# Performance work log

Measured on AMD Instinct MI355X. Metric: run time of the kernel, lower is better.

The kernel has to match this reference:

```python
import jax, jax.numpy as jnp
import numpy as np

LOCAL_RANGE = 7  # module default local_range
NUM_HEADS = 8


def setup_inputs() -> dict:
    key = jax.random.key(0)
    k1, k2, k3 = jax.random.split(key, 3)
    B, S, D = 2, 2048, 512
    hidden_states = jax.random.normal(k1, (B, S, D), dtype=jnp.float32)
    scale = 1.0 / (D ** 0.5)
    Wq = jax.random.normal(k2, (D, D), dtype=jnp.float32) * scale
    Wk = jax.random.normal(k3, (D, D), dtype=jnp.float32) * scale
    return {"hidden_states": hidden_states, "Wq": Wq, "Wk": Wk}


def reference(hidden_states, Wq, Wk):
    B, S, D = hidden_states.shape
    H = NUM_HEADS
    dh = D // H
    # inner attention: only attn_weights matter (context_layer is overwritten)
    q = (hidden_states @ Wq).reshape(B, S, H, dh).transpose(0, 2, 1, 3)  # [B,H,S,dh]
    k = (hidden_states @ Wk).reshape(B, S, H, dh).transpose(0, 2, 1, 3)  # [B,H,S,dh]
    scores = jnp.einsum('bhid,bhjd->bhij', q, k) / (dh ** 0.5)          # [B,H,S,S]
    attn_weights = jax.nn.softmax(scores, axis=-1)
    # band-diagonal local mask: |i-j| <= local_range (vectorized form of the python loop)
    idx = jnp.arange(S)
    band = (jnp.abs(idx[:, None] - idx[None, :]) <= LOCAL_RANGE).astype(attn_weights.dtype)  # [S,S]
    local_w = attn_weights * band
    local_w = local_w / (jnp.sum(local_w, axis=-1, keepdims=True) + 1e-6)
    # context = matmul(local_attn_weights, hidden_states): per-head contraction
    context = jnp.einsum('bhij,bjd->bhid', local_w, hidden_states)       # [B,H,S,D]
    return context
```

## Files before the change

### kernel.cpp

```cpp
#include <hip/hip_runtime.h>
#include <hip/hip_bf16.h>
#include <math.h>

#define SEQ   2048
#define DIM   512
#define NH    8
#define DH    64
#define LR    7
#define TI    8
#define NROW  (TI + 2 * LR)

typedef __bf16 bf16_t;
typedef __bf16 bf16x8 __attribute__((ext_vector_type(8)));
typedef float  f32x4  __attribute__((ext_vector_type(4)));

typedef __attribute__((address_space(3))) void  lds_void;
typedef __attribute__((address_space(1))) const void gbl_cvoid;

__global__ __launch_bounds__(256) void prep(
    const float* __restrict__ hs,
    const float* __restrict__ Wq, const float* __restrict__ Wk,
    bf16_t* __restrict__ hsb,
    bf16_t* __restrict__ Wt)
{
    const int tid = threadIdx.x;
    const int bx  = blockIdx.x;

    if (bx < 1024) {
        const size_t base = ((size_t)bx * 256 + tid) * 8;
        const float4 f0 = *(const float4*)(hs + base);
        const float4 f1 = *(const float4*)(hs + base + 4);
        union { bf16_t b[8]; uint4 u; } cv;
        cv.b[0]=(bf16_t)f0.x; cv.b[1]=(bf16_t)f0.y; cv.b[2]=(bf16_t)f0.z; cv.b[3]=(bf16_t)f0.w;
        cv.b[4]=(bf16_t)f1.x; cv.b[5]=(bf16_t)f1.y; cv.b[6]=(bf16_t)f1.z; cv.b[7]=(bf16_t)f1.w;
        *(uint4*)(hsb + base) = cv.u;
        return;
    }

    __shared__ float tile[64][68];
    const int t  = bx - 1024;
    const int k0 = (t & 7) * 64;
    const int n0 = (t >> 3) * 64;
    const float* W = (n0 < DIM) ? Wq : Wk;
    const int nn0 = n0 & (DIM - 1);

    #pragma unroll
    for (int ph = 0; ph < 4; ++ph) {
        const int kk = ph * 16 + (tid >> 4);
        const int nn = (tid & 15) * 4;
        const float4 v = *(const float4*)(W + (size_t)(k0 + kk) * DIM + nn0 + nn);
        tile[kk][nn + 0] = v.x; tile[kk][nn + 1] = v.y;
        tile[kk][nn + 2] = v.z; tile[kk][nn + 3] = v.w;
    }
    __syncthreads();
    #pragma unroll
    for (int ph = 0; ph < 4; ++ph) {
        const int nn = ph * 16 + (tid >> 4);
        const int kk = (tid & 15) * 4;
        union { bf16_t b[4]; ushort4 u; } cv;
        #pragma unroll
        for (int u = 0; u < 4; ++u) cv.b[u] = (bf16_t)tile[kk + u][nn];
        *(ushort4*)(Wt + (size_t)(n0 + nn) * DIM + k0 + kk) = cv.u;
    }
}

__global__ __launch_bounds__(256) void qk_gemm_v5(
    const bf16_t* __restrict__ A,
    const bf16_t* __restrict__ Bt,
    bf16_t* __restrict__ C)
{
    __shared__ bf16_t As[128 * 128];
    __shared__ bf16_t Bs[128 * 128];

    const int tid  = threadIdx.x;
    const int wave = tid >> 6;
    const int lane = tid & 63;
    const int l15  = lane & 15;
    const int quad = lane >> 4;
    const int wm   = (wave >> 1) * 64;
    const int wn_  = (wave & 1) * 64;
    const int m0   = blockIdx.x * 128;
    const int n0   = blockIdx.y * 128;

    f32x4 acc[4][4] = {};

    for (int kt = 0; kt < 4; ++kt) {
        const int k0 = kt * 128;
        #pragma unroll
        for (int g = 0; g < 8; ++g) {
            const int ra = wave * 32 + g * 4 + quad;
            const int cg = (l15 ^ (ra & 15)) * 8;
            __builtin_amdgcn_global_load_lds(
                (gbl_cvoid*)(A + (size_t)(m0 + ra) * DIM + k0 + cg),
                (lds_void*)(As + (wave * 32 + g * 4) * 128), 16, 0, 0);
            __builtin_amdgcn_global_load_lds(
                (gbl_cvoid*)(Bt + (size_t)(n0 + ra) * DIM + k0 + cg),
                (lds_void*)(Bs + (wave * 32 + g * 4) * 128), 16, 0, 0);
        }
        __syncthreads();

        #pragma unroll
        for (int s = 0; s < 4; ++s) {
            const int cs = ((s * 4 + quad) ^ l15) * 8;
            bf16x8 af[4], bfv[4];
            #pragma unroll
            for (int mi = 0; mi < 4; ++mi)
                af[mi] = *(const bf16x8*)(As + (wm + mi * 16 + l15) * 128 + cs);
            #pragma unroll
            for (int ni = 0; ni < 4; ++ni)
                bfv[ni] = *(const bf16x8*)(Bs + (wn_ + ni * 16 + l15) * 128 + cs);
            #pragma unroll
            for (int mi = 0; mi < 4; ++mi)
                #pragma unroll
                for (int ni = 0; ni < 4; ++ni)
                    acc[mi][ni] = __builtin_amdgcn_mfma_f32_16x16x32_bf16(
                        af[mi], bfv[ni], acc[mi][ni], 0, 0, 0);
        }
        __syncthreads();
    }

    bf16_t* Ct = As;
    #pragma unroll
    for (int mi = 0; mi < 4; ++mi)
        #pragma unroll
        for (int ni = 0; ni < 4; ++ni)
            #pragma unroll
            for (int r = 0; r < 4; ++r)
                Ct[(wm + mi * 16 + quad * 4 + r) * 128 + wn_ + ni * 16 + l15] =
                    (bf16_t)acc[mi][ni][r];
    __syncthreads();
    #pragma unroll
    for (int i = 0; i < 8; ++i) {
        const int idx = i * 256 + tid;
        const int row = idx >> 4;
        const int c16 = idx & 15;
        *(uint4*)(C + (size_t)(m0 + row) * 1024 + n0 + c16 * 8) =
            *(const uint4*)(Ct + row * 128 + c16 * 8);
    }
}

#define QS 520

__global__ __launch_bounds__(256) void scores_k(
    const bf16_t* __restrict__ qkb,
    float* __restrict__ wn_g)
{
    __shared__ bf16_t Qb[16 * QS];
    __shared__ bf16_t Kb[32 * QS];
    __shared__ float sw2[NH][TI][24];

    const int tid  = threadIdx.x;
    const int wave = tid >> 6;
    const int lane = tid & 63;
    const int l15  = lane & 15;
    const int quad = lane >> 4;
    const int i0   = blockIdx.x * TI;
    const int b    = blockIdx.y;

    for (int r = wave; r < TI; r += 4) {
        const bf16_t* g = qkb + (size_t)(b * SEQ + i0 + r) * 1024 + lane * 8;
        __builtin_amdgcn_global_load_lds((gbl_cvoid*)g, (lds_void*)(Qb + r * QS), 16, 0, 0);
    }
    for (int r = wave; r < NROW; r += 4) {
        int jg = i0 - LR + r;
        jg = jg < 0 ? 0 : (jg > SEQ - 1 ? SEQ - 1 : jg);
        const bf16_t* g = qkb + (size_t)(b * SEQ + jg) * 1024 + DIM + lane * 8;
        __builtin_amdgcn_global_load_lds((gbl_cvoid*)g, (lds_void*)(Kb + r * QS), 16, 0, 0);
    }
    __syncthreads();

    #pragma unroll
    for (int hh = 0; hh < 2; ++hh) {
        const int h = wave * 2 + hh;
        f32x4 sacc[2] = {};
        #pragma unroll
        for (int s = 0; s < 2; ++s) {
            const bf16x8 aq = *(const bf16x8*)(Qb + l15 * QS + h * DH + s * 32 + quad * 8);
            #pragma unroll
            for (int t = 0; t < 2; ++t) {
                const bf16x8 bk = *(const bf16x8*)(Kb + (t * 16 + l15) * QS + h * DH + s * 32 + quad * 8);
                sacc[t] = __builtin_amdgcn_mfma_f32_16x16x32_bf16(aq, bk, sacc[t], 0, 0, 0);
            }
        }
        #pragma unroll
        for (int t = 0; t < 2; ++t) {
            const int jj = t * 16 + l15;
            if (jj < NROW) {
                #pragma unroll
                for (int r = 0; r < 4; ++r) {
                    const int ii = quad * 4 + r;
                    if (ii < TI) sw2[h][ii][jj] = sacc[t][r] * 0.125f;
                }
            }
        }
    }
    __syncthreads();

    if (tid < NH * TI) {
        const int h  = tid >> 3;
        const int ii = tid & (TI - 1);
        const int i  = i0 + ii;
        float v[16], m = -1e30f;
        #pragma unroll
        for (int t = 0; t < 15; ++t) {
            const int jg = i - LR + t;
            v[t] = (jg >= 0 && jg < SEQ) ? sw2[h][ii][ii + t] : -1e30f;
            m = fmaxf(m, v[t]);
        }
        float sum = 0.f;
        #pragma unroll
        for (int t = 0; t < 15; ++t) { v[t] = __expf(v[t] - m); sum += v[t]; }
        const float inv = 1.f / sum;
        #pragma unroll
        for (int t = 0; t < 15; ++t) v[t] *= inv;
        v[15] = 0.f;
        float* dst = wn_g + ((size_t)(b * 256 + blockIdx.x) * 64 + tid) * 16;
        #pragma unroll
        for (int u = 0; u < 4; ++u)
            *(float4*)(dst + u * 4) = make_float4(v[u*4], v[u*4+1], v[u*4+2], v[u*4+3]);
    }
}

#define BST 260

__global__ __launch_bounds__(256) void context_k(
    const float* __restrict__ hs,
    const float* __restrict__ wn_g,
    float* __restrict__ out)
{
    __shared__ float band[NROW * BST];
    __shared__ float wnl[64 * 16];

    const int tid  = threadIdx.x;
    const int wave = tid >> 6;
    const int lane = tid & 63;
    const int tile = blockIdx.x;
    const int dh_  = blockIdx.y;
    const int b    = blockIdx.z;
    const int i0   = tile * TI;

    for (int r = wave; r < NROW; r += 4) {
        int jg = i0 - LR + r;
        jg = jg < 0 ? 0 : (jg > SEQ - 1 ? SEQ - 1 : jg);
        const float* g = hs + ((size_t)b * SEQ + jg) * DIM + dh_ * 256 + lane * 4;
        __builtin_amdgcn_global_load_lds((gbl_cvoid*)g, (lds_void*)(band + r * BST), 16, 0, 0);
    }
    {
        const float* g = wn_g + (size_t)(b * 256 + tile) * 1024 + wave * 256 + lane * 4;
        __builtin_amdgcn_global_load_lds((gbl_cvoid*)g, (lds_void*)(wnl + wave * 256), 16, 0, 0);
    }
    __syncthreads();

    const int h  = tid >> 5;
    const int iq = (tid >> 4) & 1;
    const int dg = tid & 15;

    float wreg[4][15];
    #pragma unroll
    for (int t = 0; t < 4; ++t) {
        const int pair = h * TI + iq * 4 + t;
        #pragma unroll
        for (int j = 0; j < 15; ++j) wreg[t][j] = wnl[pair * 16 + j];
    }

    const int r0 = iq * 4;
    float* op = out + ((size_t)(b * NH + h) * SEQ + i0 + iq * 4) * DIM + dh_ * 256;

    for (int c = 0; c < 4; ++c) {
        const int dbase = c * 64 + dg * 4;
        float4 a0 = {0,0,0,0}, a1 = {0,0,0,0}, a2 = {0,0,0,0}, a3 = {0,0,0,0};
        #pragma unroll
        for (int rr = 0; rr < 18; ++rr) {
            const float4 v = *(const float4*)&band[(r0 + rr) * BST + dbase];
            if (rr <= 14) {
                const float w = wreg[0][rr];
                a0.x += w * v.x; a0.y += w * v.y; a0.z += w * v.z; a0.w += w * v.w;
            }
            if (rr >= 1 && rr <= 15) {
                const float w = wreg[1][rr - 1];
                a1.x += w * v.x; a1.y += w * v.y; a1.z += w * v.z; a1.w += w * v.w;
            }
            if (rr >= 2 && rr <= 16) {
                const float w = wreg[2][rr - 2];
                a2.x += w * v.x; a2.y += w * v.y; a2.z += w * v.z; a2.w += w * v.w;
            }
            if (rr >= 3) {
                const float w = wreg[3][rr - 3];
                a3.x += w * v.x; a3.y += w * v.y; a3.z += w * v.z; a3.w += w * v.w;
            }
        }
        *(float4*)(op + (size_t)0 * DIM + dbase) = a0;
        *(float4*)(op + (size_t)1 * DIM + dbase) = a1;
        *(float4*)(op + (size_t)2 * DIM + dbase) = a2;
        *(float4*)(op + (size_t)3 * DIM + dbase) = a3;
    }
}

extern "C" void kernel_launch(void* const* d_in, const int* in_sizes, int n_in,
                              void* d_out, int out_size, void* d_ws, size_t ws_size,
                              hipStream_t stream)
{
    const float* hs = (const float*)d_in[0];
    const float* Wq = (const float*)d_in[1];
    const float* Wk = (const float*)d_in[2];
    float* out = (float*)d_out;

    const int B = in_sizes[0] / (SEQ * DIM);
    const int M = B * SEQ;

    bf16_t* hsb  = (bf16_t*)d_ws;
    bf16_t* Wt   = (bf16_t*)((char*)d_ws + (4 << 20));
    bf16_t* qkb  = (bf16_t*)((char*)d_ws + (5 << 20));
    float*  wn_g = (float*)((char*)d_ws + (13 << 20));

    prep<<<1024 + 128, 256, 0, stream>>>(hs, Wq, Wk, hsb, Wt);
    qk_gemm_v5<<<dim3(M / 128, 1024 / 128), 256, 0, stream>>>(hsb, Wt, qkb);
    scores_k<<<dim3(SEQ / TI, B), 256, 0, stream>>>(qkb, wn_g);
    context_k<<<dim3(SEQ / TI, 2, B), 256, 0, stream>>>(hs, wn_g, out);
}
```

Before: 109.0 us.

## Shrink QK GEMM tiles to 64x64 with smaller LDS footprint for occupancy

Replaces the 128x128-tile QK projection GEMM with a 64x64-tile version using a 64-wide k step and a flat 1D grid of four times as many blocks. LDS use drops from 64KB to 16KB per block, so more blocks can be resident per CU and the 256-block grid no longer underfills the device. The XOR swizzle is dropped and per-wave MFMA reuse is lower, which may add LDS bank conflicts and more global traffic per FLOP.

Measured after the change: 107.7 us. No clear change (-1.3%).

```diff
diff --git a/kernel.cpp b/kernel.cpp
--- a/kernel.cpp
+++ b/kernel.cpp
@@ -64,78 +64,86 @@
     }
 }
 
-__global__ __launch_bounds__(256) void qk_gemm_v5(
+__global__ __launch_bounds__(256) void qk_gemm_v6(
     const bf16_t* __restrict__ A,
     const bf16_t* __restrict__ Bt,
     bf16_t* __restrict__ C)
 {
-    __shared__ bf16_t As[128 * 128];
-    __shared__ bf16_t Bs[128 * 128];
+    __shared__ bf16_t S[4 * 64 * 32];
+    bf16_t* As0 = S;
+    bf16_t* As1 = S + 2048;
+    bf16_t* Bs0 = S + 4096;
+    bf16_t* Bs1 = S + 6144;
 
     const int tid  = threadIdx.x;
     const int wave = tid >> 6;
     const int lane = tid & 63;
     const int l15  = lane & 15;
     const int quad = lane >> 4;
-    const int wm   = (wave >> 1) * 64;
-    const int wn_  = (wave & 1) * 64;
-    const int m0   = blockIdx.x * 128;
-    const int n0   = blockIdx.y * 128;
-
-    f32x4 acc[4][4] = {};
-
-    for (int kt = 0; kt < 4; ++kt) {
-        const int k0 = kt * 128;
-        #pragma unroll
-        for (int g = 0; g < 8; ++g) {
-            const int ra = wave * 32 + g * 4 + quad;
-            const int cg = (l15 ^ (ra & 15)) * 8;
-            __builtin_amdgcn_global_load_lds(
-                (gbl_cvoid*)(A + (size_t)(m0 + ra) * DIM + k0 + cg),
-                (lds_void*)(As + (wave * 32 + g * 4) * 128), 16, 0, 0);
-            __builtin_amdgcn_global_load_lds(
-                (gbl_cvoid*)(Bt + (size_t)(n0 + ra) * DIM + k0 + cg),
-                (lds_void*)(Bs + (wave * 32 + g * 4) * 128), 16, 0, 0);
-        }
+    const int bid  = blockIdx.x;
+    const int m0   = (bid & 63) * 64;
+    const int n0   = (bid >> 6) * 64;
+    const int wm   = (wave >> 1) * 32;
+    const int wn_  = (wave & 1) * 32;
+
+    const int srow = lane >> 2;
+    const int scol = (lane & 3) * 8;
+
+    const bf16_t* agp = A  + (size_t)(m0 + wave * 16 + srow) * DIM + scol;
+    const bf16_t* bgp = Bt + (size_t)(n0 + wave * 16 + srow) * DIM + scol;
+    bf16_t* al0 = As0 + wave * 16 * 32;
+    bf16_t* al1 = As1 + wave * 16 * 32;
+    bf16_t* bl0 = Bs0 + wave * 16 * 32;
+    bf16_t* bl1 = Bs1 + wave * 16 * 32;
+
+    f32x4 acc[2][2] = {};
+
+    for (int k0 = 0; k0 < DIM; k0 += 64) {
+        __builtin_amdgcn_global_load_lds((gbl_cvoid*)(agp + k0),      (lds_void*)al0, 16, 0, 0);
+        __builtin_amdgcn_global_load_lds((gbl_cvoid*)(agp + k0 + 32), (lds_void*)al1, 16, 0, 0);
+        __builtin_amdgcn_global_load_lds((gbl_cvoid*)(bgp + k0),      (lds_void*)bl0, 16, 0, 0);
+        __builtin_amdgcn_global_load_lds((gbl_cvoid*)(bgp + k0 + 32), (lds_void*)bl1, 16, 0, 0);
         __syncthreads();
 
         #pragma unroll
-        for (int s = 0; s < 4; ++s) {
-            const int cs = ((s * 4 + quad) ^ l15) * 8;
-            bf16x8 af[4], bfv[4];
-            #pragma unroll
-            for (int mi = 0; mi < 4; ++mi)
-                af[mi] = *(const bf16x8*)(As + (wm + mi * 16 + l15) * 128 + cs);
-            #pragma unroll
-            for (int ni = 0; ni < 4; ++ni)
-                bfv[ni] = *(const bf16x8*)(Bs + (wn_ + ni * 16 + l15) * 128 + cs);
-            #pragma unroll
-            for (int mi = 0; mi < 4; ++mi)
+        for (int s = 0; s < 2; ++s) {
+            const bf16_t* PA = s ? As1 : As0;
+            const bf16_t* PB = s ? Bs1 : Bs0;
+            bf16x8 af[2], bfv[2];
+            #pragma unroll
+            for (int mi = 0; mi < 2; ++mi)
+                af[mi] = *(const bf16x8*)(PA + (wm + mi * 16 + l15) * 32 + quad * 8);
+            #pragma unroll
+            for (int ni = 0; ni < 2; ++ni)
+                bfv[ni] = *(const bf16x8*)(PB + (wn_ + ni * 16 + l15) * 32 + quad * 8);
+            #pragma unroll
+            for (int mi = 0; mi < 2; ++mi)
                 #pragma unroll
-                for (int ni = 0; ni < 4; ++ni)
+                for (int ni = 0; ni < 2; ++ni)
                     acc[mi][ni] = __builtin_amdgcn_mfma_f32_16x16x32_bf16(
                         af[mi], bfv[ni], acc[mi][ni], 0, 0, 0);
         }
         __syncthreads();
     }
 
-    bf16_t* Ct = As;
-    #pragma unroll
-    for (int mi = 0; mi < 4; ++mi)
-        #pragma unroll
-        for (int ni = 0; ni < 4; ++ni)
+    bf16_t* Ct = S;
+    #pragma unroll
+    for (int mi = 0; mi < 2; ++mi)
+        #pragma unroll
+        for (int ni = 0; ni < 2; ++ni)
             #pragma unroll
             for (int r = 0; r < 4; ++r)
-                Ct[(wm + mi * 16 + quad * 4 + r) * 128 + wn_ + ni * 16 + l15] =
+                Ct[(wm + mi * 16 + quad * 4 + r) * 64 + wn_ + ni * 16 + l15] =
                     (bf16_t)acc[mi][ni][r];
     __syncthreads();
     #pragma unroll
-    for (int i = 0; i < 8; ++i) {
+    for (int i = 0; i < 4; ++i) {
         const int idx = i * 256 + tid;
-        const int row = idx >> 4;
-        const int c16 = idx & 15;
-        *(uint4*)(C + (size_t)(m0 + row) * 1024 + n0 + c16 * 8) =
-            *(const uint4*)(Ct + row * 128 + c16 * 8);
+        const int row = idx >> 3;
+        const int c8  = idx & 7;
+        if (row < 64)
+            *(uint4*)(C + (size_t)(m0 + row) * 1024 + n0 + c8 * 8) =
+                *(const uint4*)(Ct + row * 64 + c8 * 8);
     }
 }
 
@@ -314,7 +322,7 @@
     float*  wn_g = (float*)((char*)d_ws + (13 << 20));
 
     prep<<<1024 + 128, 256, 0, stream>>>(hs, Wq, Wk, hsb, Wt);
-    qk_gemm_v5<<<dim3(M / 128, 1024 / 128), 256, 0, stream>>>(hsb, Wt, qkb);
+    qk_gemm_v6<<<(M / 64) * (1024 / 64), 256, 0, stream>>>(hsb, Wt, qkb);
     scores_k<<<dim3(SEQ / TI, B), 256, 0, stream>>>(qkb, wn_g);
     context_k<<<dim3(SEQ / TI, 2, B), 256, 0, stream>>>(hs, wn_g, out);
 }
```
